# Kernel optimization log

Measured on AMD Instinct MI355X. Metric: run time of the kernel, lower is better.

Reference implementation:

```python
import jax, jax.numpy as jnp
import numpy as np

N_NODES = 100_000
N_EDGES = 1_600_000
F_NODE = 16
F_EDGE = 8
HID = 128
N_GRAPHS = 2048


def setup_inputs() -> dict:
    key = jax.random.key(0)
    ks = jax.random.split(key, 20)
    inp = {
        "node_attr": jax.random.normal(ks[0], (N_NODES, F_NODE), dtype=jnp.float32),
        "edge_attr": jax.random.normal(ks[1], (N_EDGES, F_EDGE), dtype=jnp.float32),
        "edge_index": jax.random.randint(ks[2], (2, N_EDGES), 0, N_NODES),
        "adj_index": jax.random.randint(ks[3], (2, N_EDGES), 0, N_NODES),
        "adj_value": jax.random.uniform(ks[4], (N_EDGES,), dtype=jnp.float32) * 0.1,
        "batch": jnp.sort(jax.random.randint(ks[5], (N_NODES,), 0, N_GRAPHS)),
    }
    def glorot(k, shape):
        fan_in, fan_out = shape[0], shape[1]
        std = jnp.sqrt(2.0 / (fan_in + fan_out)).astype(jnp.float32)
        return jax.random.normal(k, shape, dtype=jnp.float32) * std
    # attr embedder params
    inp["W_node"] = glorot(ks[6], (F_NODE, HID))
    inp["W_edge"] = glorot(ks[7], (F_EDGE, HID))
    inp["b_embed"] = jnp.zeros((HID,), dtype=jnp.float32)
    # 3 GCN layers
    inp["W1"] = glorot(ks[8], (HID, HID)); inp["b1"] = jnp.zeros((HID,), jnp.float32)
    inp["W2"] = glorot(ks[9], (HID, HID)); inp["b2"] = jnp.zeros((HID,), jnp.float32)
    inp["W3"] = glorot(ks[10], (HID, HID)); inp["b3"] = jnp.zeros((HID,), jnp.float32)
    # predictor MLP
    inp["Wp1"] = glorot(ks[11], (HID, HID)); inp["bp1"] = jnp.full((HID,), 0.01, jnp.float32)
    inp["Wp2"] = glorot(ks[12], (HID, 1));   inp["bp2"] = jnp.full((1,), 0.01, jnp.float32)
    return inp


def _forward(node_attr, edge_attr, adj_value,
             W_node, W_edge, b_embed, W1, b1, W2, b2, W3, b3,
             Wp1, bp1, Wp2, bp2, edge_index, adj_index, batch):
    # --- attr embedder: mix node feats with edge feats scattered to dst nodes ---
    he = edge_attr @ W_edge                                   # [E, H]
    agg = jax.ops.segment_sum(he, edge_index[1], num_segments=N_NODES)
    h = jax.nn.relu(node_attr @ W_node + agg + b_embed)       # [N, H]

    # --- GCN stack: h <- relu(tilde_A @ (h W) + b) via sparse COO SpMM ---
    src, dst = adj_index[0], adj_index[1]
    def gcn(h, W, b):
        hw = h @ W + b                                        # [N, H]
        msg = adj_value[:, None] * hw[dst]                    # [E, H] gather
        return jax.nn.relu(jax.ops.segment_sum(msg, src, num_segments=N_NODES))
    h = gcn(h, W1, b1)
    h = gcn(h, W2, b2)
    h = gcn(h, W3, b3)

    # --- global_add_pool over graphs ---
    fp = jax.ops.segment_sum(h, batch, num_segments=N_GRAPHS)  # [G, H]

    # --- predictor MLP ---
    z = jax.nn.relu(fp @ Wp1 + bp1)
    return z @ Wp2 + bp2                                       # [G, 1]


def reference(node_attr, edge_attr, edge_index, adj_index, adj_value, batch,
              W_node, W_edge, b_embed, W1, b1, W2, b2, W3, b3,
              Wp1, bp1, Wp2, bp2):
    return _forward(node_attr, edge_attr, adj_value,
                    W_node, W_edge, b_embed, W1, b1, W2, b2, W3, b3,
                    Wp1, bp1, Wp2, bp2, edge_index, adj_index, batch)
```

## Files before the change

kernel.cpp:

```cpp
#include <hip/hip_runtime.h>

#define H 128
#define FN 16
#define FE 8
#define NBUK_MAX 1600

__global__ __launch_bounds__(256) void k_hist2_gb(
    const int* __restrict__ k1, const int* __restrict__ k2,
    int* __restrict__ bcnt1, int* __restrict__ bcnt2, int E, int nbuk,
    const int* __restrict__ batch, int* __restrict__ gstart, int N, int G) {
  if (blockIdx.x >= 512) {
    int n = (blockIdx.x - 512) * 256 + threadIdx.x;
    if (n > N) return;
    if (n == 0) {
      for (int g = 0; g <= batch[0]; g++) gstart[g] = 0;
    } else if (n == N) {
      for (int g = batch[N - 1] + 1; g <= G; g++) gstart[g] = N;
    } else {
      int b0 = batch[n - 1], b1 = batch[n];
      for (int g = b0 + 1; g <= b1; g++) gstart[g] = n;
    }
    return;
  }
  __shared__ int h1[NBUK_MAX], h2[NBUK_MAX];
  for (int i = threadIdx.x; i < nbuk; i += 256) { h1[i] = 0; h2[i] = 0; }
  __syncthreads();
  for (int e = blockIdx.x * 256 + threadIdx.x; e < E; e += 512 * 256) {
    atomicAdd(&h1[k1[e] >> 6], 1);
    atomicAdd(&h2[k2[e] >> 6], 1);
  }
  __syncthreads();
  for (int i = threadIdx.x; i < nbuk; i += 256) {
    if (h1[i]) atomicAdd(&bcnt1[i], h1[i]);
    if (h2[i]) atomicAdd(&bcnt2[i], h2[i]);
  }
}

__global__ __launch_bounds__(1024) void k_scan(
    const int* __restrict__ cnt1, int* __restrict__ st1, int* __restrict__ gc1,
    const int* __restrict__ cnt2, int* __restrict__ st2, int* __restrict__ gc2,
    int nbuk) {
  __shared__ int s[1024];
  int tid = threadIdx.x;
  for (int pass = 0; pass < 2; pass++) {
    const int* cnt = pass ? cnt2 : cnt1;
    int* st = pass ? st2 : st1;
    int* gc = pass ? gc2 : gc1;
    int run = 0;
    for (int half = 0; half * 1024 < nbuk; half++) {
      int i = half * 1024 + tid;
      int v = (i < nbuk) ? cnt[i] : 0;
      s[tid] = v; __syncthreads();
      for (int off = 1; off < 1024; off <<= 1) {
        int t = (tid >= off) ? s[tid - off] : 0;
        __syncthreads();
        s[tid] += t;
        __syncthreads();
      }
      int excl = run + s[tid] - v;
      if (i < nbuk) { st[i] = excl; gc[i] = excl; }
      run += s[1023];
      __syncthreads();
    }
    if (tid == 0) st[nbuk] = run;
    __syncthreads();
  }
}

__global__ __launch_bounds__(256) void k_p1_both(
    const int* __restrict__ k1, const int* __restrict__ adj, const float* __restrict__ vals,
    int* __restrict__ gcur1, int* __restrict__ gcur2,
    int* __restrict__ pkey, int2* __restrict__ bpay, int E, int nbuk, int p1b) {
  __shared__ int hc[NBUK_MAX];
  int tid = threadIdx.x;
  bool packed = (int)blockIdx.x < p1b;
  int chunk = packed ? blockIdx.x : blockIdx.x - p1b;
  const int* key = packed ? k1 : adj;
  int* gcur = packed ? gcur1 : gcur2;
  int c0 = chunk * 8192;
  int c1 = min(c0 + 8192, E);
  for (int i = tid; i < nbuk; i += 256) hc[i] = 0;
  __syncthreads();
  for (int e = c0 + tid; e < c1; e += 256)
    atomicAdd(&hc[key[e] >> 6], 1);
  __syncthreads();
  for (int i = tid; i < nbuk; i += 256) {
    int c = hc[i];
    if (c) hc[i] = atomicAdd(&gcur[i], c);
  }
  __syncthreads();
  if (packed) {
    for (int e = c0 + tid; e < c1; e += 256) {
      int k = key[e];
      int pos = atomicAdd(&hc[k >> 6], 1);
      pkey[pos] = (e << 6) | (k & 63);
    }
  } else {
    const int* dsts = adj + E;
    for (int e = c0 + tid; e < c1; e += 256) {
      int k = key[e];
      int pos = atomicAdd(&hc[k >> 6], 1);
      bpay[pos] = make_int2(dsts[e] | ((k & 63) << 20), __float_as_int(vals[e]));
    }
  }
}

__global__ __launch_bounds__(256) void k_agg_p2(
    const int* __restrict__ pkey, const float* __restrict__ edge_attr,
    const int* __restrict__ bst1, float* __restrict__ agg8,
    const int2* __restrict__ bpay, const int* __restrict__ bst2,
    int* __restrict__ offs, int2* __restrict__ payF, float* __restrict__ rs,
    int N, int E, int nbuk) {
  __shared__ float lds[FE][64];
  __shared__ int cnt[64], scn[64], cur[64];
  __shared__ float vsum[64];
  int tid = threadIdx.x;

  if ((int)blockIdx.x < nbuk) {
    int b = blockIdx.x;
    for (int i = tid; i < FE * 64; i += 256) ((float*)lds)[i] = 0.f;
    __syncthreads();
    int s = bst1[b], t = bst1[b + 1];
    int i = s + tid;
    for (; i + 256 < t; i += 512) {
      int pk0 = pkey[i], pk1 = pkey[i + 256];
      const float4* e0 = (const float4*)(edge_attr + (size_t)(pk0 >> 6) * FE);
      const float4* e1 = (const float4*)(edge_attr + (size_t)(pk1 >> 6) * FE);
      float4 a0 = e0[0], b0 = e0[1], a1 = e1[0], b1 = e1[1];
      int s0 = pk0 & 63, s1 = pk1 & 63;
      atomicAdd(&lds[0][s0], a0.x);  atomicAdd(&lds[1][s0], a0.y);
      atomicAdd(&lds[2][s0], a0.z);  atomicAdd(&lds[3][s0], a0.w);
      atomicAdd(&lds[4][s0], b0.x);  atomicAdd(&lds[5][s0], b0.y);
      atomicAdd(&lds[6][s0], b0.z);  atomicAdd(&lds[7][s0], b0.w);
      atomicAdd(&lds[0][s1], a1.x);  atomicAdd(&lds[1][s1], a1.y);
      atomicAdd(&lds[2][s1], a1.z);  atomicAdd(&lds[3][s1], a1.w);
      atomicAdd(&lds[4][s1], b1.x);  atomicAdd(&lds[5][s1], b1.y);
      atomicAdd(&lds[6][s1], b1.z);  atomicAdd(&lds[7][s1], b1.w);
    }
    for (; i < t; i += 256) {
      int pk = pkey[i];
      int e = pk >> 6, slot = pk & 63;
      const float4* ea = (const float4*)(edge_attr + (size_t)e * FE);
      float4 a = ea[0], b4 = ea[1];
      atomicAdd(&lds[0][slot], a.x);  atomicAdd(&lds[1][slot], a.y);
      atomicAdd(&lds[2][slot], a.z);  atomicAdd(&lds[3][slot], a.w);
      atomicAdd(&lds[4][slot], b4.x); atomicAdd(&lds[5][slot], b4.y);
      atomicAdd(&lds[6][slot], b4.z); atomicAdd(&lds[7][slot], b4.w);
    }
    __syncthreads();
    int node0 = b * 64;
    for (int j = tid; j < 64 * FE; j += 256) {
      int n = node0 + (j >> 3);
      if (n < N) agg8[(size_t)n * FE + (j & 7)] = lds[j & 7][j >> 3];
    }
  } else {
    int b = blockIdx.x - nbuk;
    int s = bst2[b], t = bst2[b + 1];
    if (tid < 64) { cnt[tid] = 0; vsum[tid] = 0.f; }
    __syncthreads();
    for (int i = s + tid; i < t; i += 256) atomicAdd(&cnt[(bpay[i].x >> 20) & 63], 1);
    __syncthreads();
    if (tid < 64) scn[tid] = cnt[tid];
    __syncthreads();
    for (int off = 1; off < 64; off <<= 1) {
      int v = 0;
      if (tid < 64 && tid >= off) v = scn[tid - off];
      __syncthreads();
      if (tid < 64 && tid >= off) scn[tid] += v;
      __syncthreads();
    }
    if (tid < 64) {
      int excl = s + scn[tid] - cnt[tid];
      cur[tid] = excl;
      int node = b * 64 + tid;
      if (node < N) offs[node] = excl;
    }
    if (b == 0 && tid == 0) offs[N] = E;
    __syncthreads();
    for (int i = s + tid; i < t; i += 256) {
      int2 p = bpay[i];
      int slot = (p.x >> 20) & 63;
      int pos = atomicAdd(&cur[slot], 1);
      payF[pos] = make_int2(p.x & 0xFFFFF, p.y);
      atomicAdd(&vsum[slot], __int_as_float(p.y));
    }
    __syncthreads();
    if (tid < 64) {
      int node = b * 64 + tid;
      if (node < N) rs[node] = vsum[tid];
    }
  }
}

__global__ __launch_bounds__(256) void k_embed_h(
    const float* __restrict__ node_attr, const float* __restrict__ Wn,
    const float* __restrict__ We8, const float* __restrict__ b,
    const float* __restrict__ agg8, float* __restrict__ h, int N) {
  __shared__ float Ws[FN * H];
  __shared__ float Es[FE * H];
  __shared__ float na[2][FN];
  __shared__ float a8[2][FE];
  for (int i = threadIdx.x; i < FN * H; i += 256) Ws[i] = Wn[i];
  for (int i = threadIdx.x; i < FE * H; i += 256) Es[i] = We8[i];
  int lane = threadIdx.x & 127;
  int sub  = threadIdx.x >> 7;
  for (int n0 = blockIdx.x * 2; n0 < N; n0 += gridDim.x * 2) {
    int n = n0 + sub;
    __syncthreads();
    if (n < N) {
      if (lane < FN) na[sub][lane] = node_attr[(size_t)n * FN + lane];
      else if (lane < FN + FE) a8[sub][lane - FN] = agg8[(size_t)n * FE + (lane - FN)];
    }
    __syncthreads();
    if (n < N) {
      float acc = b[lane];
#pragma unroll
      for (int k = 0; k < FN; k++) acc += na[sub][k] * Ws[k * H + lane];
#pragma unroll
      for (int k = 0; k < FE; k++) acc += a8[sub][k] * Es[k * H + lane];
      h[(size_t)n * H + lane] = fmaxf(acc, 0.f);
    }
  }
}

__global__ __launch_bounds__(512, 8) void k_fused(
    const float* __restrict__ h, const int* __restrict__ offs,
    const int2* __restrict__ pay, const float* __restrict__ W,
    const float* __restrict__ bias, const float* __restrict__ rs,
    float* __restrict__ out, int N) {
  __shared__ float4 hs4[64 * 32];
  int tid = threadIdx.x;
  int c  = tid & 31;
  int rg = tid >> 5;
  int base = blockIdx.x * 64;
  const float4* h4 = (const float4*)h;

  for (int r = 0; r < 4; r++) {
    int row = rg * 4 + r;
    int n = base + row;
    float4 a0 = make_float4(0.f, 0.f, 0.f, 0.f);
    float4 a1 = make_float4(0.f, 0.f, 0.f, 0.f);
    float4 a2 = make_float4(0.f, 0.f, 0.f, 0.f);
    float4 a3 = make_float4(0.f, 0.f, 0.f, 0.f);
    if (n < N) {
      int s = offs[n], t = offs[n + 1];
      int i = s, t4 = s + ((t - s) & ~3);
      for (; i < t4; i += 4) {
        int2 p0 = pay[i], p1 = pay[i + 1], p2 = pay[i + 2], p3 = pay[i + 3];
        float4 h0 = h4[(size_t)p0.x * 32 + c];
        float4 h1 = h4[(size_t)p1.x * 32 + c];
        float4 h2 = h4[(size_t)p2.x * 32 + c];
        float4 h3 = h4[(size_t)p3.x * 32 + c];
        float v0 = __int_as_float(p0.y), v1 = __int_as_float(p1.y);
        float v2 = __int_as_float(p2.y), v3 = __int_as_float(p3.y);
        a0.x += v0 * h0.x; a0.y += v0 * h0.y; a0.z += v0 * h0.z; a0.w += v0 * h0.w;
        a1.x += v1 * h1.x; a1.y += v1 * h1.y; a1.z += v1 * h1.z; a1.w += v1 * h1.w;
        a2.x += v2 * h2.x; a2.y += v2 * h2.y; a2.z += v2 * h2.z; a2.w += v2 * h2.w;
        a3.x += v3 * h3.x; a3.y += v3 * h3.y; a3.z += v3 * h3.z; a3.w += v3 * h3.w;
      }
      for (; i < t; i++) {
        int2 p = pay[i];
        float v = __int_as_float(p.y);
        float4 hv = h4[(size_t)p.x * 32 + c];
        a0.x += v * hv.x; a0.y += v * hv.y; a0.z += v * hv.z; a0.w += v * hv.w;
      }
    }
    hs4[row * 32 + c] = make_float4(a0.x + a1.x + a2.x + a3.x,
                                    a0.y + a1.y + a2.y + a3.y,
                                    a0.z + a1.z + a2.z + a3.z,
                                    a0.w + a1.w + a2.w + a3.w);
  }
  __syncthreads();

  const float4* W4 = (const float4*)W;
  float4 acc[4];
#pragma unroll
  for (int i = 0; i < 4; i++) acc[i] = make_float4(0.f, 0.f, 0.f, 0.f);
#pragma unroll 2
  for (int k = 0; k < 32; k++) {
    float4 w0 = W4[(k * 4 + 0) * 32 + c];
    float4 w1 = W4[(k * 4 + 1) * 32 + c];
    float4 w2 = W4[(k * 4 + 2) * 32 + c];
    float4 w3 = W4[(k * 4 + 3) * 32 + c];
#pragma unroll
    for (int i = 0; i < 4; i++) {
      float4 hv = hs4[(rg + 16 * i) * 32 + k];
      acc[i].x += hv.x * w0.x + hv.y * w1.x + hv.z * w2.x + hv.w * w3.x;
      acc[i].y += hv.x * w0.y + hv.y * w1.y + hv.z * w2.y + hv.w * w3.y;
      acc[i].z += hv.x * w0.z + hv.y * w1.z + hv.z * w2.z + hv.w * w3.z;
      acc[i].w += hv.x * w0.w + hv.y * w1.w + hv.z * w2.w + hv.w * w3.w;
    }
  }

  float4 bv = ((const float4*)bias)[c];
#pragma unroll
  for (int i = 0; i < 4; i++) {
    int row = rg + 16 * i;
    int n = base + row;
    if (n < N) {
      float rsv = rs[n];
      float4 o;
      o.x = fmaxf(acc[i].x + rsv * bv.x, 0.f);
      o.y = fmaxf(acc[i].y + rsv * bv.y, 0.f);
      o.z = fmaxf(acc[i].z + rsv * bv.z, 0.f);
      o.w = fmaxf(acc[i].w + rsv * bv.w, 0.f);
      ((float4*)out)[(size_t)n * 32 + c] = o;
    }
  }
}

__global__ __launch_bounds__(256) void k_gemm_pred(
    const float* __restrict__ in, const float* __restrict__ W,
    const float* __restrict__ bias, const float* __restrict__ Wp2,
    const float* __restrict__ bp2, float* __restrict__ out, int N) {
  __shared__ float4 hs4[64 * 32];
  int tid = threadIdx.x;
  int c  = tid & 31;
  int rg = tid >> 5;
  int rowBase = blockIdx.x * 64;
  const float4* in4 = (const float4*)in;
  const float4* W4  = (const float4*)W;
#pragma unroll
  for (int j = 0; j < 8; j++) {
    int q = tid + 256 * j;
    int r = rowBase + (q >> 5);
    int rr = (r < N) ? r : (N - 1);
    hs4[q] = in4[(size_t)rr * 32 + (q & 31)];
  }
  __syncthreads();
  float4 acc[8];
#pragma unroll
  for (int i = 0; i < 8; i++) acc[i] = make_float4(0.f, 0.f, 0.f, 0.f);
#pragma unroll 2
  for (int k = 0; k < 32; k++) {
    float4 w0 = W4[(k * 4 + 0) * 32 + c];
    float4 w1 = W4[(k * 4 + 1) * 32 + c];
    float4 w2 = W4[(k * 4 + 2) * 32 + c];
    float4 w3 = W4[(k * 4 + 3) * 32 + c];
#pragma unroll
    for (int i = 0; i < 8; i++) {
      float4 hv = hs4[(rg + 8 * i) * 32 + k];
      acc[i].x += hv.x * w0.x + hv.y * w1.x + hv.z * w2.x + hv.w * w3.x;
      acc[i].y += hv.x * w0.y + hv.y * w1.y + hv.z * w2.y + hv.w * w3.y;
      acc[i].z += hv.x * w0.z + hv.y * w1.z + hv.z * w2.z + hv.w * w3.z;
      acc[i].w += hv.x * w0.w + hv.y * w1.w + hv.z * w2.w + hv.w * w3.w;
    }
  }
  float4 bv = ((const float4*)bias)[c];
  float4 wp = ((const float4*)Wp2)[c];
  float bp = bp2[0];
#pragma unroll
  for (int i = 0; i < 8; i++) {
    int row = rowBase + rg + 8 * i;
    float4 o;
    o.x = fmaxf(acc[i].x + bv.x, 0.f);
    o.y = fmaxf(acc[i].y + bv.y, 0.f);
    o.z = fmaxf(acc[i].z + bv.z, 0.f);
    o.w = fmaxf(acc[i].w + bv.w, 0.f);
    float v = o.x * wp.x + o.y * wp.y + o.z * wp.z + o.w * wp.w;
#pragma unroll
    for (int off = 16; off > 0; off >>= 1) v += __shfl_down(v, off, 32);
    if (c == 0 && row < N) out[row] = v + bp;
  }
}

__global__ __launch_bounds__(256) void k_pool_seg(
    const float* __restrict__ h, const int* __restrict__ gstart,
    float* __restrict__ fp, int G) {
  __shared__ float4 red[8][32];
  int g = blockIdx.x;
  int c = threadIdx.x & 31, rg = threadIdx.x >> 5;
  int s = gstart[g], t = gstart[g + 1];
  const float4* h4 = (const float4*)h;
  float4 a = make_float4(0.f, 0.f, 0.f, 0.f);
  for (int n = s + rg; n < t; n += 8) {
    float4 v = h4[(size_t)n * 32 + c];
    a.x += v.x; a.y += v.y; a.z += v.z; a.w += v.w;
  }
  red[rg][c] = a;
  __syncthreads();
  if (rg == 0) {
    float4 r = red[0][c];
#pragma unroll
    for (int j = 1; j < 8; j++) {
      float4 v = red[j][c];
      r.x += v.x; r.y += v.y; r.z += v.z; r.w += v.w;
    }
    ((float4*)fp)[(size_t)g * 32 + c] = r;
  }
}

extern "C" void kernel_launch(void* const* d_in, const int* in_sizes, int n_in,
                              void* d_out, int out_size, void* d_ws, size_t ws_size,
                              hipStream_t stream) {
  const float* node_attr  = (const float*)d_in[0];
  const float* edge_attr  = (const float*)d_in[1];
  const int*   edge_index = (const int*)d_in[2];
  const int*   adj_index  = (const int*)d_in[3];
  const float* adj_value  = (const float*)d_in[4];
  const int*   batch      = (const int*)d_in[5];
  const float* W_node  = (const float*)d_in[6];
  const float* W_edge  = (const float*)d_in[7];
  const float* b_embed = (const float*)d_in[8];
  const float* W1 = (const float*)d_in[9];
  const float* b1 = (const float*)d_in[10];
  const float* W2 = (const float*)d_in[11];
  const float* b2 = (const float*)d_in[12];
  const float* W3 = (const float*)d_in[13];
  const float* b3 = (const float*)d_in[14];
  const float* Wp1 = (const float*)d_in[15];
  const float* bp1 = (const float*)d_in[16];
  const float* Wp2 = (const float*)d_in[17];
  const float* bp2 = (const float*)d_in[18];
  float* out = (float*)d_out;

  const int E = in_sizes[4];
  const int N = in_sizes[5];
  const int G = out_size;
  const int nbuk = (N + 63) >> 6;
  const int p1b = (E + 8191) / 8192;
  const int gbB = (N + 256) / 256;

  float* A     = (float*)d_ws;
  float* B     = A + (size_t)N * H;
  int2*  payF  = (int2*)(B + (size_t)N * H);
  float* fpool = (float*)(payF + E);
  int*   bcnt1 = (int*)(fpool + (size_t)G * H);
  int*   bcnt2 = bcnt1 + nbuk;
  int*   bst1  = bcnt2 + nbuk;
  int*   gcur1 = bst1 + nbuk + 1;
  int*   bst2  = gcur1 + nbuk;
  int*   gcur2 = bst2 + nbuk + 1;
  int*   offs2 = gcur2 + nbuk;
  int*   gstart= offs2 + N + 1;
  float* rs    = (float*)(gstart + G + 1);
  float* agg8  = A;
  int*   pkey  = (int*)B;
  int2*  bpay2 = (int2*)(((int*)B) + E);

  hipMemsetAsync(bcnt1, 0, (size_t)2 * nbuk * sizeof(int), stream);
  k_hist2_gb<<<512 + gbB, 256, 0, stream>>>(edge_index + E, adj_index, bcnt1, bcnt2,
                                            E, nbuk, batch, gstart, N, G);
  k_scan<<<1, 1024, 0, stream>>>(bcnt1, bst1, gcur1, bcnt2, bst2, gcur2, nbuk);

  k_p1_both<<<2 * p1b, 256, 0, stream>>>(edge_index + E, adj_index, adj_value,
                                         gcur1, gcur2, pkey, bpay2, E, nbuk, p1b);

  k_agg_p2<<<2 * nbuk, 256, 0, stream>>>(pkey, edge_attr, bst1, agg8,
                                         bpay2, bst2, offs2, payF, rs, N, E, nbuk);

  k_embed_h<<<4096, 256, 0, stream>>>(node_attr, W_node, W_edge, b_embed, agg8, B, N);

  int lb = (N + 63) / 64;
  k_fused<<<lb, 512, 0, stream>>>(B, offs2, payF, W1, b1, rs, A, N);
  k_fused<<<lb, 512, 0, stream>>>(A, offs2, payF, W2, b2, rs, B, N);
  k_fused<<<lb, 512, 0, stream>>>(B, offs2, payF, W3, b3, rs, A, N);

  k_pool_seg<<<G, 256, 0, stream>>>(A, gstart, fpool, G);
  k_gemm_pred<<<(G + 63) / 64, 256, 0, stream>>>(fpool, Wp1, bp1, Wp2, bp2, out, G);
}
```

Baseline: 955.1 us.

## Fuse node embedding into edge aggregation kernel and shrink GCN block size

Merges the embedding GEMV (node_attr@W_node + agg@W_edge + bias, relu) into the bucketed edge-aggregation kernel, so the per-node 8-wide aggregate stays in LDS and h is written directly to buffer A. This drops one launch and the agg8 round trip through global memory. The fused GCN kernel also moves from 512-thread/64-row blocks to 256-thread/32-row blocks for finer granularity, and the ping-pong buffers are swapped to match. In exchange, the aggregation blocks carry 24 weight registers per thread plus a 32-iteration output loop.

```diff
diff --git a/kernel.cpp b/kernel.cpp
--- a/kernel.cpp
+++ b/kernel.cpp
@@ -107,18 +107,36 @@
 
 __global__ __launch_bounds__(256) void k_agg_p2(
     const int* __restrict__ pkey, const float* __restrict__ edge_attr,
-    const int* __restrict__ bst1, float* __restrict__ agg8,
+    const int* __restrict__ bst1,
+    const float* __restrict__ node_attr, const float* __restrict__ Wn,
+    const float* __restrict__ We8, const float* __restrict__ bemb,
+    float* __restrict__ hout,
     const int2* __restrict__ bpay, const int* __restrict__ bst2,
     int* __restrict__ offs, int2* __restrict__ payF, float* __restrict__ rs,
     int N, int E, int nbuk) {
   __shared__ float lds[FE][64];
+  __shared__ float na[64][FN];
   __shared__ int cnt[64], scn[64], cur[64];
   __shared__ float vsum[64];
   int tid = threadIdx.x;
 
   if ((int)blockIdx.x < nbuk) {
     int b = blockIdx.x;
+    int node0 = b * 64;
+    int col = tid & 127;
+    int half = tid >> 7;
+    float wreg[FN + FE];
+#pragma unroll
+    for (int k = 0; k < FN; k++) wreg[k] = Wn[k * H + col];
+#pragma unroll
+    for (int k = 0; k < FE; k++) wreg[FN + k] = We8[k * H + col];
+    float bcol = bemb[col];
+
     for (int i = tid; i < FE * 64; i += 256) ((float*)lds)[i] = 0.f;
+    for (int i = tid; i < 64 * FN; i += 256) {
+      int n = node0 + (i >> 4);
+      na[i >> 4][i & 15] = (n < N) ? node_attr[(size_t)n * FN + (i & 15)] : 0.f;
+    }
     __syncthreads();
     int s = bst1[b], t = bst1[b + 1];
     int i = s + tid;
@@ -148,10 +166,15 @@
       atomicAdd(&lds[6][slot], b4.z); atomicAdd(&lds[7][slot], b4.w);
     }
     __syncthreads();
-    int node0 = b * 64;
-    for (int j = tid; j < 64 * FE; j += 256) {
-      int n = node0 + (j >> 3);
-      if (n < N) agg8[(size_t)n * FE + (j & 7)] = lds[j & 7][j >> 3];
+    for (int pr = 0; pr < 32; pr++) {
+      int nl = pr * 2 + half;
+      int n = node0 + nl;
+      float acc = bcol;
+#pragma unroll
+      for (int k = 0; k < FN; k++) acc += na[nl][k] * wreg[k];
+#pragma unroll
+      for (int k = 0; k < FE; k++) acc += lds[k][nl] * wreg[FN + k];
+      if (n < N) hout[(size_t)n * H + col] = fmaxf(acc, 0.f);
     }
   } else {
     int b = blockIdx.x - nbuk;
@@ -192,47 +215,16 @@
   }
 }
 
-__global__ __launch_bounds__(256) void k_embed_h(
-    const float* __restrict__ node_attr, const float* __restrict__ Wn,
-    const float* __restrict__ We8, const float* __restrict__ b,
-    const float* __restrict__ agg8, float* __restrict__ h, int N) {
-  __shared__ float Ws[FN * H];
-  __shared__ float Es[FE * H];
-  __shared__ float na[2][FN];
-  __shared__ float a8[2][FE];
-  for (int i = threadIdx.x; i < FN * H; i += 256) Ws[i] = Wn[i];
-  for (int i = threadIdx.x; i < FE * H; i += 256) Es[i] = We8[i];
-  int lane = threadIdx.x & 127;
-  int sub  = threadIdx.x >> 7;
-  for (int n0 = blockIdx.x * 2; n0 < N; n0 += gridDim.x * 2) {
-    int n = n0 + sub;
-    __syncthreads();
-    if (n < N) {
-      if (lane < FN) na[sub][lane] = node_attr[(size_t)n * FN + lane];
-      else if (lane < FN + FE) a8[sub][lane - FN] = agg8[(size_t)n * FE + (lane - FN)];
-    }
-    __syncthreads();
-    if (n < N) {
-      float acc = b[lane];
-#pragma unroll
-      for (int k = 0; k < FN; k++) acc += na[sub][k] * Ws[k * H + lane];
-#pragma unroll
-      for (int k = 0; k < FE; k++) acc += a8[sub][k] * Es[k * H + lane];
-      h[(size_t)n * H + lane] = fmaxf(acc, 0.f);
-    }
-  }
-}
-
-__global__ __launch_bounds__(512, 8) void k_fused(
+__global__ __launch_bounds__(256, 8) void k_fused(
     const float* __restrict__ h, const int* __restrict__ offs,
     const int2* __restrict__ pay, const float* __restrict__ W,
     const float* __restrict__ bias, const float* __restrict__ rs,
     float* __restrict__ out, int N) {
-  __shared__ float4 hs4[64 * 32];
+  __shared__ float4 hs4[32 * 32];
   int tid = threadIdx.x;
   int c  = tid & 31;
   int rg = tid >> 5;
-  int base = blockIdx.x * 64;
+  int base = blockIdx.x * 32;
   const float4* h4 = (const float4*)h;
 
   for (int r = 0; r < 4; r++) {
@@ -284,7 +276,7 @@
     float4 w3 = W4[(k * 4 + 3) * 32 + c];
 #pragma unroll
     for (int i = 0; i < 4; i++) {
-      float4 hv = hs4[(rg + 16 * i) * 32 + k];
+      float4 hv = hs4[(rg + 8 * i) * 32 + k];
       acc[i].x += hv.x * w0.x + hv.y * w1.x + hv.z * w2.x + hv.w * w3.x;
       acc[i].y += hv.x * w0.y + hv.y * w1.y + hv.z * w2.y + hv.w * w3.y;
       acc[i].z += hv.x * w0.z + hv.y * w1.z + hv.z * w2.z + hv.w * w3.z;
@@ -295,7 +287,7 @@
   float4 bv = ((const float4*)bias)[c];
 #pragma unroll
   for (int i = 0; i < 4; i++) {
-    int row = rg + 16 * i;
+    int row = rg + 8 * i;
     int n = base + row;
     if (n < N) {
       float rsv = rs[n];
@@ -434,7 +426,6 @@
   int*   offs2 = gcur2 + nbuk;
   int*   gstart= offs2 + N + 1;
   float* rs    = (float*)(gstart + G + 1);
-  float* agg8  = A;
   int*   pkey  = (int*)B;
   int2*  bpay2 = (int2*)(((int*)B) + E);
 
@@ -446,16 +437,15 @@
   k_p1_both<<<2 * p1b, 256, 0, stream>>>(edge_index + E, adj_index, adj_value,
                                          gcur1, gcur2, pkey, bpay2, E, nbuk, p1b);
 
-  k_agg_p2<<<2 * nbuk, 256, 0, stream>>>(pkey, edge_attr, bst1, agg8,
+  k_agg_p2<<<2 * nbuk, 256, 0, stream>>>(pkey, edge_attr, bst1,
+                                         node_attr, W_node, W_edge, b_embed, A,
                                          bpay2, bst2, offs2, payF, rs, N, E, nbuk);
 
-  k_embed_h<<<4096, 256, 0, stream>>>(node_attr, W_node, W_edge, b_embed, agg8, B, N);
-
-  int lb = (N + 63) / 64;
-  k_fused<<<lb, 512, 0, stream>>>(B, offs2, payF, W1, b1, rs, A, N);
-  k_fused<<<lb, 512, 0, stream>>>(A, offs2, payF, W2, b2, rs, B, N);
-  k_fused<<<lb, 512, 0, stream>>>(B, offs2, payF, W3, b3, rs, A, N);
-
-  k_pool_seg<<<G, 256, 0, stream>>>(A, gstart, fpool, G);
+  int lb = (N + 31) / 32;
+  k_fused<<<lb, 256, 0, stream>>>(A, offs2, payF, W1, b1, rs, B, N);
+  k_fused<<<lb, 256, 0, stream>>>(B, offs2, payF, W2, b2, rs, A, N);
+  k_fused<<<lb, 256, 0, stream>>>(A, offs2, payF, W3, b3, rs, B, N);
+
+  k_pool_seg<<<G, 256, 0, stream>>>(B, gstart, fpool, G);
   k_gemm_pred<<<(G + 63) / 64, 256, 0, stream>>>(fpool, Wp1, bp1, Wp2, bp2, out, G);
 }
```

Result: faster. 888.1 us (-7.0%).
